# Performance work log

Hardware: AMD Instinct MI355X
Metric: run time of the kernel (lower is better)

Reference implementation:

```python
import jax, jax.numpy as jnp
import numpy as np

B, N, C, P, K = 8, 65536, 96, 96, 512


def _ln(x, g, b, eps=1e-5):
    mu = x.mean(axis=-1, keepdims=True)
    var = ((x - mu) ** 2).mean(axis=-1, keepdims=True)
    return (x - mu) * jax.lax.rsqrt(var + eps) * g + b


def setup_inputs():
    key = jax.random.key(0)
    ks = jax.random.split(key, 8)
    inp = {
        "pts_feat": jax.random.normal(ks[0], (B, N, C), jnp.float32),
        "sp_idx": jax.random.randint(ks[1], (B, N), 0, K, jnp.int64),
        "all_xyz": jax.random.normal(ks[2], (B, N, 3), jnp.float32),
        # pts_proj1: Linear(3,P) -> LN -> ReLU -> Linear(P,P) -> LN
        "W1": jax.random.normal(ks[3], (3, P), jnp.float32) / np.sqrt(3.0),
        "b1": jnp.zeros((P,), jnp.float32),
        "g1": jnp.ones((P,), jnp.float32),
        "be1": jnp.zeros((P,), jnp.float32),
        "W2": jax.random.normal(ks[4], (P, P), jnp.float32) / np.sqrt(P),
        "b2": jnp.zeros((P,), jnp.float32),
        "g2": jnp.ones((P,), jnp.float32),
        "be2": jnp.zeros((P,), jnp.float32),
        # pts_proj2: Linear(2P,P) -> LN -> ReLU -> Linear(P,1,no bias) -> Sigmoid
        "W3": jax.random.normal(ks[5], (2 * P, P), jnp.float32) / np.sqrt(2.0 * P),
        "b3": jnp.zeros((P,), jnp.float32),
        "g3": jnp.ones((P,), jnp.float32),
        "be3": jnp.zeros((P,), jnp.float32),
        "W4": jax.random.normal(ks[6], (P, 1), jnp.float32) / np.sqrt(P),
        "num_sp": K,
    }
    return inp


def reference(pts_feat, sp_idx, all_xyz, W1, b1, g1, be1, W2, b2, g2, be2,
              W3, b3, g3, be3, W4, num_sp):
    Bx, Nx, Cx = pts_feat.shape
    S = Bx * num_sp  # total superpoints across batch (uniform K per batch)
    idx = (sp_idx + jnp.arange(Bx, dtype=sp_idx.dtype)[:, None] * num_sp).reshape(-1)
    xyz = all_xyz.reshape(-1, 3)
    feat = pts_feat.reshape(-1, Cx)

    # scatter_norm: unit-sphere normalize per segment
    mn = jax.ops.segment_min(xyz, idx, num_segments=S)
    mx = jax.ops.segment_max(xyz, idx, num_segments=S)
    cnt = jax.ops.segment_sum(jnp.ones((xyz.shape[0],), xyz.dtype), idx, num_segments=S)
    cnt_c = jnp.maximum(cnt, 1.0)
    center = jax.ops.segment_sum(xyz, idx, num_segments=S) / cnt_c[:, None]
    diam = (mx - mn).max(axis=1)
    pts = (xyz - center[idx]) / (diam[idx][:, None] + 0.01)

    # pts_proj1
    h = _ln(pts @ W1 + b1, g1, be1)
    h = jax.nn.relu(h)
    h = _ln(h @ W2 + b2, g2, be2)

    seg = jax.ops.segment_max(h, idx, num_segments=S)  # (S, P)
    cat = jnp.concatenate([h, seg[idx]], axis=-1)      # (B*N, 2P)

    # pts_proj2
    z = _ln(cat @ W3 + b3, g3, be3)
    z = jax.nn.relu(z)
    w = jax.nn.sigmoid(z @ W4) * 2.0                   # (B*N, 1)

    sp_feat = jax.ops.segment_sum(feat * w, idx, num_segments=S) / cnt_c[:, None] + seg
    return sp_feat.reshape(Bx, num_sp, Cx), w.reshape(Bx, Nx, 1)
```

## Files before the change

### kernel.cpp

```cpp
#include <hip/hip_runtime.h>
#include <cstdint>

#define MM 524288
#define NSEG 4096

#define WS_SCNT   0u
#define WS_CURSOR 4096u
#define WS_OFFS   8192u
#define WS_M1     12288u
#define WS_CENTER 12304u
#define WS_DIAM   24592u
#define WS_SEGF   28688u
#define WS_ZSEG   421904u
#define WS_SORTED 815120u
#define WS_SEG16  1339408u
#define WS_WSRT   1601552u
#define WS_H8     2125840u
#define WS_END    (WS_H8 + 25165824u)

typedef __attribute__((ext_vector_type(8))) short short8;
typedef __attribute__((ext_vector_type(4))) float f32x4;

#define WPAD 104

__device__ __forceinline__ unsigned bfr(float x) {
    unsigned u = __float_as_uint(x);
    return (u + 0x7FFFu + ((u >> 16) & 1u)) >> 16;
}
__device__ __forceinline__ float bf2f(unsigned v) {
    return __uint_as_float(v << 16);
}
union U4S8 { uint4 u; short8 s; };

__global__ void __launch_bounds__(256) k0_init(unsigned* __restrict__ ws)
{
    unsigned i = blockIdx.x * 256u + threadIdx.x;
    if (i < 8192u) ws[i] = 0u;
}

__global__ void __launch_bounds__(256) k1_count(
    const int* __restrict__ spidx, unsigned* __restrict__ scnt)
{
    __shared__ unsigned lcnt[512];
    int tid = threadIdx.x;
    for (int j = tid; j < 512; j += 256) lcnt[j] = 0u;
    __syncthreads();
    int base = blockIdx.x * 4096;
    #pragma unroll 4
    for (int it = 0; it < 16; ++it) {
        int p = base + it*256 + tid;
        atomicAdd(&lcnt[spidx[p]], 1u);
    }
    __syncthreads();
    int b = blockIdx.x >> 4;
    for (int j = tid; j < 512; j += 256)
        atomicAdd(&scnt[(b << 9) + j], lcnt[j]);
}

__global__ void __launch_bounds__(1024) k2_scan(
    const unsigned* __restrict__ scnt, unsigned* __restrict__ offs,
    const float* __restrict__ W1, const float* __restrict__ b1, float* __restrict__ m1)
{
    __shared__ unsigned sh[1024];
    int t = threadIdx.x;
    unsigned c0 = scnt[t*4+0], c1 = scnt[t*4+1], c2 = scnt[t*4+2], c3 = scnt[t*4+3];
    unsigned tot = c0 + c1 + c2 + c3;
    sh[t] = tot;
    __syncthreads();
    for (int d = 1; d < 1024; d <<= 1) {
        unsigned v = (t >= d) ? sh[t-d] : 0u;
        __syncthreads();
        sh[t] += v;
        __syncthreads();
    }
    unsigned excl = sh[t] - tot;
    offs[t*4+0] = excl;
    offs[t*4+1] = excl + c0;
    offs[t*4+2] = excl + c0 + c1;
    offs[t*4+3] = excl + c0 + c1 + c2;

    if (t == 0) {
        float Sa=0,Sb=0,Sc=0,Sd=0,Saa=0,Sbb=0,Scc=0,Sdd=0,Sab=0,Sac=0,Sad=0,Sbc=0,Sbd=0,Scd=0;
        #pragma unroll 8
        for (int j = 0; j < 96; ++j) {
            float A = W1[j], B2 = W1[96+j], C2 = W1[192+j], D = b1[j];
            Sa+=A; Sb+=B2; Sc+=C2; Sd+=D;
            Saa=fmaf(A,A,Saa); Sbb=fmaf(B2,B2,Sbb); Scc=fmaf(C2,C2,Scc); Sdd=fmaf(D,D,Sdd);
            Sab=fmaf(A,B2,Sab); Sac=fmaf(A,C2,Sac); Sad=fmaf(A,D,Sad);
            Sbc=fmaf(B2,C2,Sbc); Sbd=fmaf(B2,D,Sbd); Scd=fmaf(C2,D,Scd);
        }
        const float inv = 1.f/96.f;
        float Am=Sa*inv, Bm=Sb*inv, Cm=Sc*inv, Dm=Sd*inv;
        m1[0]=Am; m1[1]=Bm; m1[2]=Cm; m1[3]=Dm;
        m1[4]=Saa*inv-Am*Am; m1[5]=Sbb*inv-Bm*Bm; m1[6]=Scc*inv-Cm*Cm; m1[7]=Sdd*inv-Dm*Dm;
        m1[8]=Sab*inv-Am*Bm; m1[9]=Sac*inv-Am*Cm; m1[10]=Sad*inv-Am*Dm;
        m1[11]=Sbc*inv-Bm*Cm; m1[12]=Sbd*inv-Bm*Dm; m1[13]=Scd*inv-Cm*Dm;
    }
}

__global__ void __launch_bounds__(256) k3_scatter(
    const int* __restrict__ spidx, const unsigned* __restrict__ offs,
    unsigned* __restrict__ cursor, unsigned* __restrict__ sorted,
    unsigned short* __restrict__ seg16)
{
    __shared__ unsigned lcnt[512];
    __shared__ unsigned gbase[512];
    __shared__ unsigned short rank16[4096];
    int tid = threadIdx.x;
    for (int j = tid; j < 512; j += 256) lcnt[j] = 0u;
    __syncthreads();
    int base = blockIdx.x * 4096;
    #pragma unroll 4
    for (int it = 0; it < 16; ++it) {
        int p = base + it*256 + tid;
        unsigned r = atomicAdd(&lcnt[spidx[p]], 1u);
        rank16[it*256 + tid] = (unsigned short)r;
    }
    __syncthreads();
    int b = blockIdx.x >> 4;
    for (int j = tid; j < 512; j += 256)
        gbase[j] = atomicAdd(&cursor[(b << 9) + j], lcnt[j]);
    __syncthreads();
    #pragma unroll 4
    for (int it = 0; it < 16; ++it) {
        int p = base + it*256 + tid;
        int sl = spidx[p];
        int s = (b << 9) + sl;
        unsigned pos = offs[s] + gbase[sl] + (unsigned)rank16[it*256 + tid];
        sorted[pos] = (unsigned)p;
        seg16[pos] = (unsigned short)s;
    }
}

__global__ void __launch_bounds__(128) k3b_stats(
    const float* __restrict__ xyz, const unsigned* __restrict__ sorted,
    const unsigned* __restrict__ offs, const unsigned* __restrict__ scnt,
    float* __restrict__ center, float* __restrict__ diam)
{
    int s = blockIdx.x, tid = threadIdx.x;
    unsigned cnt = scnt[s], off = offs[s];
    float mnx=INFINITY, mny=INFINITY, mnz=INFINITY;
    float mxx=-INFINITY, mxy=-INFINITY, mxz=-INFINITY;
    float smx=0.f, smy=0.f, smz=0.f;
    for (unsigned r = tid; r < cnt; r += 128) {
        unsigned p = sorted[off + r];
        float x = xyz[3*p], y = xyz[3*p+1], z = xyz[3*p+2];
        mnx = fminf(mnx, x); mny = fminf(mny, y); mnz = fminf(mnz, z);
        mxx = fmaxf(mxx, x); mxy = fmaxf(mxy, y); mxz = fmaxf(mxz, z);
        smx += x; smy += y; smz += z;
    }
    #pragma unroll
    for (int m = 1; m < 64; m <<= 1) {
        mnx = fminf(mnx, __shfl_xor(mnx, m)); mny = fminf(mny, __shfl_xor(mny, m));
        mnz = fminf(mnz, __shfl_xor(mnz, m));
        mxx = fmaxf(mxx, __shfl_xor(mxx, m)); mxy = fmaxf(mxy, __shfl_xor(mxy, m));
        mxz = fmaxf(mxz, __shfl_xor(mxz, m));
        smx += __shfl_xor(smx, m); smy += __shfl_xor(smy, m); smz += __shfl_xor(smz, m);
    }
    __shared__ float cw[2][9];
    if ((tid & 63) == 0) {
        int w = tid >> 6;
        cw[w][0]=mnx; cw[w][1]=mny; cw[w][2]=mnz;
        cw[w][3]=mxx; cw[w][4]=mxy; cw[w][5]=mxz;
        cw[w][6]=smx; cw[w][7]=smy; cw[w][8]=smz;
    }
    __syncthreads();
    if (tid == 0) {
        float a0=fminf(cw[0][0],cw[1][0]), a1=fminf(cw[0][1],cw[1][1]), a2=fminf(cw[0][2],cw[1][2]);
        float b0=fmaxf(cw[0][3],cw[1][3]), b1=fmaxf(cw[0][4],cw[1][4]), b2=fmaxf(cw[0][5],cw[1][5]);
        float s0=cw[0][6]+cw[1][6], s1=cw[0][7]+cw[1][7], s2=cw[0][8]+cw[1][8];
        float cc = fmaxf((float)cnt, 1.f);
        center[s*3+0] = s0/cc; center[s*3+1] = s1/cc; center[s*3+2] = s2/cc;
        diam[s] = fmaxf(fmaxf(b0-a0, b1-a1), b2-a2);
    }
}

__global__ void __launch_bounds__(256) kTA(
    const float* __restrict__ xyz,
    const unsigned* __restrict__ sorted,
    const unsigned short* __restrict__ seg16,
    const float* __restrict__ center, const float* __restrict__ diam,
    const float* __restrict__ W1, const float* __restrict__ b1,
    const float* __restrict__ g1, const float* __restrict__ be1,
    const float* __restrict__ m1,
    const float* __restrict__ W2, const float* __restrict__ b2,
    const float* __restrict__ g2, const float* __restrict__ be2,
    uint4* __restrict__ h8)
{
    __shared__ unsigned short wT[96*WPAD];
    __shared__ float pw[96*6];
    __shared__ float prm[3*96];
    int tid = threadIdx.x;
    #pragma unroll 4
    for (int it = 0; it < 36; ++it) {
        int e = it*256 + tid;
        int i = e / 96, j = e - i*96;
        wT[j*WPAD + i] = (unsigned short)bfr(W2[e]);
    }
    if (tid < 96) {
        pw[tid*6+0] = W1[tid]; pw[tid*6+1] = W1[96+tid]; pw[tid*6+2] = W1[192+tid];
        pw[tid*6+3] = b1[tid]; pw[tid*6+4] = g1[tid];    pw[tid*6+5] = be1[tid];
        prm[tid] = b2[tid]; prm[96+tid] = g2[tid]; prm[192+tid] = be2[tid];
    }
    __syncthreads();

    float mc[14];
    #pragma unroll
    for (int k = 0; k < 14; ++k) mc[k] = m1[k];

    int lane = tid & 63, w = tid >> 6;
    int pcol = lane & 15, g = lane >> 4;
    size_t slot0 = (size_t)blockIdx.x * 256 + w*64 + pcol;

    #pragma unroll 1
    for (int t = 0; t < 4; ++t) {
        size_t slot = slot0 + (size_t)t * 16;
        unsigned p = sorted[slot];
        int s = seg16[slot];
        float dinv = 1.f / (diam[s] + 0.01f);
        float px = (xyz[3*p+0] - center[3*s+0]) * dinv;
        float py = (xyz[3*p+1] - center[3*s+1]) * dinv;
        float pz = (xyz[3*p+2] - center[3*s+2]) * dinv;

        float mu = fmaf(px, mc[0], fmaf(py, mc[1], fmaf(pz, mc[2], mc[3])));
        float var = fmaf(px*px, mc[4], fmaf(py*py, mc[5], fmaf(pz*pz, mc[6], mc[7])));
        var = fmaf(2.f*px*py, mc[8],  var);
        var = fmaf(2.f*px*pz, mc[9],  var);
        var = fmaf(2.f*px,    mc[10], var);
        var = fmaf(2.f*py*pz, mc[11], var);
        var = fmaf(2.f*py,    mc[12], var);
        var = fmaf(2.f*pz,    mc[13], var);
        float rs = rsqrtf(var + 1e-5f);

        U4S8 bu[3];
        #pragma unroll
        for (int ks = 0; ks < 3; ++ks) {
            unsigned vv[4];
            #pragma unroll
            for (int e2 = 0; e2 < 4; ++e2) {
                int i0 = ks*32 + g*8 + e2*2;
                const float* r0 = &pw[i0*6];
                float ta = fmaf(px, r0[0], fmaf(py, r0[1], fmaf(pz, r0[2], r0[3])));
                ta = fmaxf(fmaf((ta - mu) * rs, r0[4], r0[5]), 0.f);
                const float* r1 = &pw[(i0+1)*6];
                float tb = fmaf(px, r1[0], fmaf(py, r1[1], fmaf(pz, r1[2], r1[3])));
                tb = fmaxf(fmaf((tb - mu) * rs, r1[4], r1[5]), 0.f);
                vv[e2] = bfr(ta) | (bfr(tb) << 16);
            }
            bu[ks].u.x = vv[0]; bu[ks].u.y = vv[1]; bu[ks].u.z = vv[2]; bu[ks].u.w = vv[3];
        }

        f32x4 acc[6];
        #pragma unroll
        for (int nt = 0; nt < 6; ++nt) acc[nt] = (f32x4){0.f,0.f,0.f,0.f};

        #pragma unroll
        for (int ks = 0; ks < 3; ++ks) {
            #pragma unroll
            for (int nt = 0; nt < 6; ++nt) {
                const short8 aF = *(const short8*)&wT[(nt*16 + pcol)*WPAD + ks*32 + g*8];
                acc[nt] = __builtin_amdgcn_mfma_f32_16x16x32_bf16(aF, bu[ks].s, acc[nt], 0, 0, 0);
            }
        }

        float sum = 0.f, sq = 0.f;
        #pragma unroll
        for (int nt = 0; nt < 6; ++nt) {
            f32x4 bv = *(const f32x4*)&prm[nt*16 + g*4];
            #pragma unroll
            for (int r = 0; r < 4; ++r) {
                float v = acc[nt][r] + bv[r];
                acc[nt][r] = v;
                sum += v;
                sq = fmaf(v, v, sq);
            }
        }
        sum += __shfl_xor(sum, 16); sum += __shfl_xor(sum, 32);
        sq  += __shfl_xor(sq, 16);  sq  += __shfl_xor(sq, 32);
        float muh = sum * (1.f/96.f);
        float rsh = rsqrtf(sq * (1.f/96.f) - muh*muh + 1e-5f);

        #pragma unroll
        for (int nt = 0; nt < 6; ++nt) {
            f32x4 gv  = *(const f32x4*)&prm[96  + nt*16 + g*4];
            f32x4 bev = *(const f32x4*)&prm[192 + nt*16 + g*4];
            float o0 = fmaf((acc[nt][0]-muh)*rsh, gv[0], bev[0]);
            float o1 = fmaf((acc[nt][1]-muh)*rsh, gv[1], bev[1]);
            float o2 = fmaf((acc[nt][2]-muh)*rsh, gv[2], bev[2]);
            float o3 = fmaf((acc[nt][3]-muh)*rsh, gv[3], bev[3]);
            uint2 st;
            st.x = bfr(o0) | (bfr(o1) << 16);
            st.y = bfr(o2) | (bfr(o3) << 16);
            int j0 = nt*16 + g*4;
            size_t q = (size_t)(nt*2 + (g >> 1));
            *(uint2*)((char*)h8 + (q*MM + slot)*16 + (size_t)(j0 & 7)*2) = st;
        }
    }
}

__global__ void __launch_bounds__(192) kB_seg(
    const uint4* __restrict__ h8,
    const unsigned* __restrict__ offs, const unsigned* __restrict__ scnt,
    const float* __restrict__ W3, const float* __restrict__ b3,
    float* __restrict__ segf, float* __restrict__ zseg)
{
    __shared__ uint4 st[16][13];
    __shared__ float lseg[96];
    int s = blockIdx.x, tid = threadIdx.x;
    unsigned cnt = scnt[s], off = offs[s];
    int r = tid & 15, q = tid >> 4;
    float mx = -INFINITY;
    for (unsigned base = 0; base < cnt; base += 16) {
        uint4 v = make_uint4(0xFF80FF80u, 0xFF80FF80u, 0xFF80FF80u, 0xFF80FF80u);
        if (q < 12 && base + (unsigned)r < cnt)
            v = h8[(size_t)q * MM + off + base + r];
        if (q < 12) st[r][q] = v;
        __syncthreads();
        if (tid < 96) {
            int qj = tid >> 3, ej = tid & 7;
            #pragma unroll
            for (int rr = 0; rr < 16; ++rr) {
                const unsigned short* hp = (const unsigned short*)&st[rr][qj];
                mx = fmaxf(mx, bf2f(hp[ej]));
            }
        }
        __syncthreads();
    }
    if (tid < 96) { segf[(size_t)s*96 + tid] = mx; lseg[tid] = mx; }
    __syncthreads();
    if (tid < 96) {
        float acc = b3[tid];
        #pragma unroll 4
        for (int i = 0; i < 96; ++i)
            acc = fmaf(lseg[i], W3[(size_t)(96+i)*96 + tid], acc);
        zseg[(size_t)s*96 + tid] = acc;
    }
}

__global__ void __launch_bounds__(256) kC_mfma(
    const uint4* __restrict__ h8, const float* __restrict__ zseg,
    const unsigned short* __restrict__ seg16, const unsigned* __restrict__ sorted,
    const float* __restrict__ W3, const float* __restrict__ g3,
    const float* __restrict__ be3, const float* __restrict__ W4,
    float* __restrict__ w_nat, float* __restrict__ w_srt)
{
    __shared__ unsigned short wT[96*WPAD];
    __shared__ float prm[3*96];
    int tid = threadIdx.x;
    #pragma unroll 4
    for (int it = 0; it < 36; ++it) {
        int e = it*256 + tid;
        int i = e / 96, j = e - i*96;
        wT[j*WPAD + i] = (unsigned short)bfr(W3[e]);
    }
    if (tid < 96) { prm[tid] = g3[tid]; prm[96+tid] = be3[tid]; prm[192+tid] = W4[tid]; }
    __syncthreads();

    int lane = tid & 63, w = tid >> 6;
    int pcol = lane & 15, g = lane >> 4;
    size_t slot0 = (size_t)blockIdx.x * 256 + w*64 + pcol;

    #pragma unroll 1
    for (int t = 0; t < 4; ++t) {
        size_t slot = slot0 + (size_t)t * 16;
        U4S8 bu[3];
        #pragma unroll
        for (int ks = 0; ks < 3; ++ks)
            bu[ks].u = h8[(size_t)(ks*4+g) * MM + slot];

        f32x4 acc[6];
        #pragma unroll
        for (int nt = 0; nt < 6; ++nt) acc[nt] = (f32x4){0.f,0.f,0.f,0.f};

        #pragma unroll
        for (int ks = 0; ks < 3; ++ks) {
            #pragma unroll
            for (int nt = 0; nt < 6; ++nt) {
                const short8 aF = *(const short8*)&wT[(nt*16 + pcol)*WPAD + ks*32 + g*8];
                acc[nt] = __builtin_amdgcn_mfma_f32_16x16x32_bf16(aF, bu[ks].s, acc[nt], 0, 0, 0);
            }
        }

        int s = seg16[slot];
        float sum = 0.f, sq = 0.f;
        #pragma unroll
        for (int nt = 0; nt < 6; ++nt) {
            f32x4 zs = *(const f32x4*)&zseg[(size_t)s*96 + nt*16 + g*4];
            #pragma unroll
            for (int r = 0; r < 4; ++r) {
                float v = acc[nt][r] + zs[r];
                acc[nt][r] = v;
                sum += v;
                sq = fmaf(v, v, sq);
            }
        }
        sum += __shfl_xor(sum, 16); sum += __shfl_xor(sum, 32);
        sq  += __shfl_xor(sq, 16);  sq  += __shfl_xor(sq, 32);
        float mu = sum * (1.f/96.f);
        float rs = rsqrtf(sq * (1.f/96.f) - mu*mu + 1e-5f);

        float tt = 0.f;
        #pragma unroll
        for (int nt = 0; nt < 6; ++nt) {
            f32x4 gv  = *(const f32x4*)&prm[nt*16 + g*4];
            f32x4 bev = *(const f32x4*)&prm[96 + nt*16 + g*4];
            f32x4 w4v = *(const f32x4*)&prm[192 + nt*16 + g*4];
            #pragma unroll
            for (int r = 0; r < 4; ++r) {
                float v = fmaxf(fmaf((acc[nt][r]-mu)*rs, gv[r], bev[r]), 0.f);
                tt = fmaf(v, w4v[r], tt);
            }
        }
        tt += __shfl_xor(tt, 16); tt += __shfl_xor(tt, 32);
        if (lane < 16) {
            float wv = 2.f / (1.f + expf(-tt));
            w_srt[slot] = wv;
            w_nat[sorted[slot]] = wv;
        }
    }
}

__global__ void __launch_bounds__(128) kD_pool(
    const float* __restrict__ feat, const float* __restrict__ w_srt,
    const unsigned* __restrict__ sorted, const unsigned* __restrict__ offs,
    const unsigned* __restrict__ scnt, const float* __restrict__ segf,
    float* __restrict__ sp_out)
{
    int s = blockIdx.x;
    int c = threadIdx.x;
    unsigned cnt = scnt[s], off = offs[s];
    float acc = 0.f;
    unsigned r = 0;
    for (; r + 4 <= cnt; r += 4) {
        unsigned p0 = sorted[off+r],   p1 = sorted[off+r+1];
        unsigned p2 = sorted[off+r+2], p3 = sorted[off+r+3];
        float w0 = w_srt[off+r], w1 = w_srt[off+r+1], w2 = w_srt[off+r+2], w3 = w_srt[off+r+3];
        if (c < 96) {
            acc = fmaf(feat[(size_t)p0*96 + c], w0, acc);
            acc = fmaf(feat[(size_t)p1*96 + c], w1, acc);
            acc = fmaf(feat[(size_t)p2*96 + c], w2, acc);
            acc = fmaf(feat[(size_t)p3*96 + c], w3, acc);
        }
    }
    for (; r < cnt; ++r) {
        unsigned p0 = sorted[off+r];
        float w0 = w_srt[off+r];
        if (c < 96) acc = fmaf(feat[(size_t)p0*96 + c], w0, acc);
    }
    if (c < 96) {
        float cc = fmaxf((float)cnt, 1.f);
        sp_out[(size_t)s*96 + c] = acc / cc + segf[(size_t)s*96 + c];
    }
}

extern "C" void kernel_launch(void* const* d_in, const int* in_sizes, int n_in,
                              void* d_out, int out_size, void* d_ws, size_t ws_size,
                              hipStream_t stream)
{
    const float* pts_feat = (const float*)d_in[0];
    const int*   sp_idx   = (const int*)d_in[1];
    const float* xyz      = (const float*)d_in[2];
    const float* W1  = (const float*)d_in[3];
    const float* b1  = (const float*)d_in[4];
    const float* g1  = (const float*)d_in[5];
    const float* be1 = (const float*)d_in[6];
    const float* W2  = (const float*)d_in[7];
    const float* b2  = (const float*)d_in[8];
    const float* g2  = (const float*)d_in[9];
    const float* be2 = (const float*)d_in[10];
    const float* W3  = (const float*)d_in[11];
    const float* b3  = (const float*)d_in[12];
    const float* g3  = (const float*)d_in[13];
    const float* be3 = (const float*)d_in[14];
    const float* W4  = (const float*)d_in[15];

    float* out = (float*)d_out;
    float* sp_out = out;
    float* w_out  = out + (size_t)NSEG * 96;

    if (ws_size < (size_t)WS_END * 4u) return;

    unsigned* ws32   = (unsigned*)d_ws;
    unsigned* scnt   = ws32 + WS_SCNT;
    unsigned* cursor = ws32 + WS_CURSOR;
    unsigned* offs   = ws32 + WS_OFFS;
    float*    m1     = (float*)(ws32 + WS_M1);
    float*    center = (float*)(ws32 + WS_CENTER);
    float*    diam   = (float*)(ws32 + WS_DIAM);
    float*    segf   = (float*)(ws32 + WS_SEGF);
    float*    zseg   = (float*)(ws32 + WS_ZSEG);
    unsigned* sorted = ws32 + WS_SORTED;
    unsigned short* seg16 = (unsigned short*)(ws32 + WS_SEG16);
    float*    w_srt  = (float*)(ws32 + WS_WSRT);
    uint4*    h8     = (uint4*)(ws32 + WS_H8);

    k0_init<<<32, 256, 0, stream>>>(ws32);
    k1_count<<<MM/4096, 256, 0, stream>>>(sp_idx, scnt);
    k2_scan<<<1, 1024, 0, stream>>>(scnt, offs, W1, b1, m1);
    k3_scatter<<<MM/4096, 256, 0, stream>>>(sp_idx, offs, cursor, sorted, seg16);
    k3b_stats<<<NSEG, 128, 0, stream>>>(xyz, sorted, offs, scnt, center, diam);
    kTA<<<MM/256, 256, 0, stream>>>(xyz, sorted, seg16, center, diam,
        W1, b1, g1, be1, m1, W2, b2, g2, be2, h8);
    kB_seg<<<NSEG, 192, 0, stream>>>(h8, offs, scnt, W3, b3, segf, zseg);
    kC_mfma<<<MM/256, 256, 0, stream>>>(h8, zseg, seg16, sorted, W3, g3, be3, W4,
        w_out, w_srt);
    kD_pool<<<NSEG, 128, 0, stream>>>(pts_feat, w_srt, sorted, offs, scnt, segf, sp_out);
}
```

Baseline: 265.0 us.

## Recompute first MLP instead of storing h, fuse segment max via atomics

The bf16 intermediate h buffer (about 100 MB written and read twice) is removed. The first kernel now computes h and reduces the per-segment max in place, using order-preserving uint atomicMax into shared memory and then global memory. The second MLP kernel recomputes h from xyz and transposes it through LDS before the W3 MFMA. This trades extra MFMA and ALU work plus atomic traffic for much less HBM traffic. The pooling loop is also unrolled to 8.

```diff
diff --git a/kernel.cpp b/kernel.cpp
--- a/kernel.cpp
+++ b/kernel.cpp
@@ -10,13 +10,13 @@
 #define WS_M1     12288u
 #define WS_CENTER 12304u
 #define WS_DIAM   24592u
-#define WS_SEGF   28688u
-#define WS_ZSEG   421904u
-#define WS_SORTED 815120u
-#define WS_SEG16  1339408u
-#define WS_WSRT   1601552u
-#define WS_H8     2125840u
-#define WS_END    (WS_H8 + 25165824u)
+#define WS_SEGU   28688u
+#define WS_SEGF   421904u
+#define WS_ZSEG   815120u
+#define WS_SORTED 1208336u
+#define WS_SEG16  1732624u
+#define WS_WSRT   1994768u
+#define WS_END    2519056u
 
 typedef __attribute__((ext_vector_type(8))) short short8;
 typedef __attribute__((ext_vector_type(4))) float f32x4;
@@ -30,12 +30,21 @@
 __device__ __forceinline__ float bf2f(unsigned v) {
     return __uint_as_float(v << 16);
 }
+__device__ __forceinline__ unsigned ford(float f) {
+    unsigned u = __float_as_uint(f);
+    return (u & 0x80000000u) ? ~u : (u | 0x80000000u);
+}
+__device__ __forceinline__ float ford_inv(unsigned e) {
+    unsigned u = (e & 0x80000000u) ? (e & 0x7FFFFFFFu) : ~e;
+    return __uint_as_float(u);
+}
 union U4S8 { uint4 u; short8 s; };
 
 __global__ void __launch_bounds__(256) k0_init(unsigned* __restrict__ ws)
 {
     unsigned i = blockIdx.x * 256u + threadIdx.x;
     if (i < 8192u) ws[i] = 0u;
+    else if (i < 8192u + 393216u) ws[WS_SEGU + i - 8192u] = 0u;
 }
 
 __global__ void __launch_bounds__(256) k1_count(
@@ -175,21 +184,91 @@
     }
 }
 
-__global__ void __launch_bounds__(256) kTA(
+__device__ __forceinline__ void compute_h(
+    float px, float py, float pz, const float* mc,
+    const unsigned short* wT, const float* pw, const float* prm2,
+    int pcol, int g, f32x4 acc[6])
+{
+    float mu = fmaf(px, mc[0], fmaf(py, mc[1], fmaf(pz, mc[2], mc[3])));
+    float var = fmaf(px*px, mc[4], fmaf(py*py, mc[5], fmaf(pz*pz, mc[6], mc[7])));
+    var = fmaf(2.f*px*py, mc[8],  var);
+    var = fmaf(2.f*px*pz, mc[9],  var);
+    var = fmaf(2.f*px,    mc[10], var);
+    var = fmaf(2.f*py*pz, mc[11], var);
+    var = fmaf(2.f*py,    mc[12], var);
+    var = fmaf(2.f*pz,    mc[13], var);
+    float rs = rsqrtf(var + 1e-5f);
+
+    U4S8 bu[3];
+    #pragma unroll
+    for (int ks = 0; ks < 3; ++ks) {
+        unsigned vv[4];
+        #pragma unroll
+        for (int e2 = 0; e2 < 4; ++e2) {
+            int i0 = ks*32 + g*8 + e2*2;
+            const float* r0 = &pw[i0*6];
+            float ta = fmaf(px, r0[0], fmaf(py, r0[1], fmaf(pz, r0[2], r0[3])));
+            ta = fmaxf(fmaf((ta - mu) * rs, r0[4], r0[5]), 0.f);
+            const float* r1 = &pw[(i0+1)*6];
+            float tb = fmaf(px, r1[0], fmaf(py, r1[1], fmaf(pz, r1[2], r1[3])));
+            tb = fmaxf(fmaf((tb - mu) * rs, r1[4], r1[5]), 0.f);
+            vv[e2] = bfr(ta) | (bfr(tb) << 16);
+        }
+        bu[ks].u.x = vv[0]; bu[ks].u.y = vv[1]; bu[ks].u.z = vv[2]; bu[ks].u.w = vv[3];
+    }
+
+    #pragma unroll
+    for (int nt = 0; nt < 6; ++nt) acc[nt] = (f32x4){0.f,0.f,0.f,0.f};
+    #pragma unroll
+    for (int ks = 0; ks < 3; ++ks) {
+        #pragma unroll
+        for (int nt = 0; nt < 6; ++nt) {
+            const short8 aF = *(const short8*)&wT[(nt*16 + pcol)*WPAD + ks*32 + g*8];
+            acc[nt] = __builtin_amdgcn_mfma_f32_16x16x32_bf16(aF, bu[ks].s, acc[nt], 0, 0, 0);
+        }
+    }
+
+    float sum = 0.f, sq = 0.f;
+    #pragma unroll
+    for (int nt = 0; nt < 6; ++nt) {
+        f32x4 bv = *(const f32x4*)&prm2[nt*16 + g*4];
+        #pragma unroll
+        for (int r = 0; r < 4; ++r) {
+            float v = acc[nt][r] + bv[r];
+            acc[nt][r] = v;
+            sum += v;
+            sq = fmaf(v, v, sq);
+        }
+    }
+    sum += __shfl_xor(sum, 16); sum += __shfl_xor(sum, 32);
+    sq  += __shfl_xor(sq, 16);  sq  += __shfl_xor(sq, 32);
+    float muh = sum * (1.f/96.f);
+    float rsh = rsqrtf(sq * (1.f/96.f) - muh*muh + 1e-5f);
+    #pragma unroll
+    for (int nt = 0; nt < 6; ++nt) {
+        f32x4 gv  = *(const f32x4*)&prm2[96  + nt*16 + g*4];
+        f32x4 bev = *(const f32x4*)&prm2[192 + nt*16 + g*4];
+        #pragma unroll
+        for (int r = 0; r < 4; ++r)
+            acc[nt][r] = fmaf((acc[nt][r]-muh)*rsh, gv[r], bev[r]);
+    }
+}
+
+__global__ void __launch_bounds__(256) kS_segmax(
     const float* __restrict__ xyz,
-    const unsigned* __restrict__ sorted,
-    const unsigned short* __restrict__ seg16,
+    const unsigned* __restrict__ sorted, const unsigned short* __restrict__ seg16,
     const float* __restrict__ center, const float* __restrict__ diam,
     const float* __restrict__ W1, const float* __restrict__ b1,
     const float* __restrict__ g1, const float* __restrict__ be1,
     const float* __restrict__ m1,
     const float* __restrict__ W2, const float* __restrict__ b2,
     const float* __restrict__ g2, const float* __restrict__ be2,
-    uint4* __restrict__ h8)
+    unsigned* __restrict__ segu)
 {
     __shared__ unsigned short wT[96*WPAD];
     __shared__ float pw[96*6];
-    __shared__ float prm[3*96];
+    __shared__ float prm2[3*96];
+    __shared__ unsigned lmax[8*96];
     int tid = threadIdx.x;
     #pragma unroll 4
     for (int it = 0; it < 36; ++it) {
@@ -200,8 +279,9 @@
     if (tid < 96) {
         pw[tid*6+0] = W1[tid]; pw[tid*6+1] = W1[96+tid]; pw[tid*6+2] = W1[192+tid];
         pw[tid*6+3] = b1[tid]; pw[tid*6+4] = g1[tid];    pw[tid*6+5] = be1[tid];
-        prm[tid] = b2[tid]; prm[96+tid] = g2[tid]; prm[192+tid] = be2[tid];
-    }
+        prm2[tid] = b2[tid]; prm2[96+tid] = g2[tid]; prm2[192+tid] = be2[tid];
+    }
+    for (int k = tid; k < 768; k += 256) lmax[k] = 0u;
     __syncthreads();
 
     float mc[14];
@@ -211,122 +291,90 @@
     int lane = tid & 63, w = tid >> 6;
     int pcol = lane & 15, g = lane >> 4;
     size_t slot0 = (size_t)blockIdx.x * 256 + w*64 + pcol;
+    int s0 = seg16[(size_t)blockIdx.x * 256];
 
     #pragma unroll 1
     for (int t = 0; t < 4; ++t) {
         size_t slot = slot0 + (size_t)t * 16;
         unsigned p = sorted[slot];
-        int s = seg16[slot];
-        float dinv = 1.f / (diam[s] + 0.01f);
-        float px = (xyz[3*p+0] - center[3*s+0]) * dinv;
-        float py = (xyz[3*p+1] - center[3*s+1]) * dinv;
-        float pz = (xyz[3*p+2] - center[3*s+2]) * dinv;
-
-        float mu = fmaf(px, mc[0], fmaf(py, mc[1], fmaf(pz, mc[2], mc[3])));
-        float var = fmaf(px*px, mc[4], fmaf(py*py, mc[5], fmaf(pz*pz, mc[6], mc[7])));
-        var = fmaf(2.f*px*py, mc[8],  var);
-        var = fmaf(2.f*px*pz, mc[9],  var);
-        var = fmaf(2.f*px,    mc[10], var);
-        var = fmaf(2.f*py*pz, mc[11], var);
-        var = fmaf(2.f*py,    mc[12], var);
-        var = fmaf(2.f*pz,    mc[13], var);
-        float rs = rsqrtf(var + 1e-5f);
-
-        U4S8 bu[3];
-        #pragma unroll
-        for (int ks = 0; ks < 3; ++ks) {
-            unsigned vv[4];
+        int ss = seg16[slot];
+        float dinv = 1.f / (diam[ss] + 0.01f);
+        float px = (xyz[3*p+0] - center[3*ss+0]) * dinv;
+        float py = (xyz[3*p+1] - center[3*ss+1]) * dinv;
+        float pz = (xyz[3*p+2] - center[3*ss+2]) * dinv;
+
+        f32x4 acc[6];
+        compute_h(px, py, pz, mc, wT, pw, prm2, pcol, g, acc);
+
+        int smin = ss, smax = ss;
+        #pragma unroll
+        for (int m = 1; m < 16; m <<= 1) {
+            smin = min(smin, __shfl_xor(smin, m));
+            smax = max(smax, __shfl_xor(smax, m));
+        }
+        if (smin == smax) {
             #pragma unroll
-            for (int e2 = 0; e2 < 4; ++e2) {
-                int i0 = ks*32 + g*8 + e2*2;
-                const float* r0 = &pw[i0*6];
-                float ta = fmaf(px, r0[0], fmaf(py, r0[1], fmaf(pz, r0[2], r0[3])));
-                ta = fmaxf(fmaf((ta - mu) * rs, r0[4], r0[5]), 0.f);
-                const float* r1 = &pw[(i0+1)*6];
-                float tb = fmaf(px, r1[0], fmaf(py, r1[1], fmaf(pz, r1[2], r1[3])));
-                tb = fmaxf(fmaf((tb - mu) * rs, r1[4], r1[5]), 0.f);
-                vv[e2] = bfr(ta) | (bfr(tb) << 16);
+            for (int m = 1; m < 16; m <<= 1)
+                #pragma unroll
+                for (int nt = 0; nt < 6; ++nt)
+                    #pragma unroll
+                    for (int rr = 0; rr < 4; ++rr)
+                        acc[nt][rr] = fmaxf(acc[nt][rr], __shfl_xor(acc[nt][rr], m));
+            if (pcol == 0) {
+                int rel = ss - s0;
+                if (rel < 8) {
+                    #pragma unroll
+                    for (int nt = 0; nt < 6; ++nt)
+                        #pragma unroll
+                        for (int rr = 0; rr < 4; ++rr)
+                            atomicMax(&lmax[rel*96 + nt*16 + g*4 + rr], ford(acc[nt][rr]));
+                } else {
+                    #pragma unroll
+                    for (int nt = 0; nt < 6; ++nt)
+                        #pragma unroll
+                        for (int rr = 0; rr < 4; ++rr)
+                            atomicMax(&segu[(size_t)ss*96 + nt*16 + g*4 + rr], ford(acc[nt][rr]));
+                }
             }
-            bu[ks].u.x = vv[0]; bu[ks].u.y = vv[1]; bu[ks].u.z = vv[2]; bu[ks].u.w = vv[3];
-        }
-
-        f32x4 acc[6];
-        #pragma unroll
-        for (int nt = 0; nt < 6; ++nt) acc[nt] = (f32x4){0.f,0.f,0.f,0.f};
-
-        #pragma unroll
-        for (int ks = 0; ks < 3; ++ks) {
+        } else {
+            int rel = ss - s0;
             #pragma unroll
             for (int nt = 0; nt < 6; ++nt) {
-                const short8 aF = *(const short8*)&wT[(nt*16 + pcol)*WPAD + ks*32 + g*8];
-                acc[nt] = __builtin_amdgcn_mfma_f32_16x16x32_bf16(aF, bu[ks].s, acc[nt], 0, 0, 0);
+                #pragma unroll
+                for (int rr = 0; rr < 4; ++rr) {
+                    unsigned e = ford(acc[nt][rr]);
+                    int j = nt*16 + g*4 + rr;
+                    if (rel < 8) atomicMax(&lmax[rel*96 + j], e);
+                    else         atomicMax(&segu[(size_t)ss*96 + j], e);
+                }
             }
         }
-
-        float sum = 0.f, sq = 0.f;
-        #pragma unroll
-        for (int nt = 0; nt < 6; ++nt) {
-            f32x4 bv = *(const f32x4*)&prm[nt*16 + g*4];
-            #pragma unroll
-            for (int r = 0; r < 4; ++r) {
-                float v = acc[nt][r] + bv[r];
-                acc[nt][r] = v;
-                sum += v;
-                sq = fmaf(v, v, sq);
-            }
-        }
-        sum += __shfl_xor(sum, 16); sum += __shfl_xor(sum, 32);
-        sq  += __shfl_xor(sq, 16);  sq  += __shfl_xor(sq, 32);
-        float muh = sum * (1.f/96.f);
-        float rsh = rsqrtf(sq * (1.f/96.f) - muh*muh + 1e-5f);
-
-        #pragma unroll
-        for (int nt = 0; nt < 6; ++nt) {
-            f32x4 gv  = *(const f32x4*)&prm[96  + nt*16 + g*4];
-            f32x4 bev = *(const f32x4*)&prm[192 + nt*16 + g*4];
-            float o0 = fmaf((acc[nt][0]-muh)*rsh, gv[0], bev[0]);
-            float o1 = fmaf((acc[nt][1]-muh)*rsh, gv[1], bev[1]);
-            float o2 = fmaf((acc[nt][2]-muh)*rsh, gv[2], bev[2]);
-            float o3 = fmaf((acc[nt][3]-muh)*rsh, gv[3], bev[3]);
-            uint2 st;
-            st.x = bfr(o0) | (bfr(o1) << 16);
-            st.y = bfr(o2) | (bfr(o3) << 16);
-            int j0 = nt*16 + g*4;
-            size_t q = (size_t)(nt*2 + (g >> 1));
-            *(uint2*)((char*)h8 + (q*MM + slot)*16 + (size_t)(j0 & 7)*2) = st;
-        }
-    }
-}
-
-__global__ void __launch_bounds__(192) kB_seg(
-    const uint4* __restrict__ h8,
-    const unsigned* __restrict__ offs, const unsigned* __restrict__ scnt,
+    }
+    __syncthreads();
+    for (int k = tid; k < 768; k += 256) {
+        unsigned v = lmax[k];
+        if (v) {
+            int rel = k / 96, j = k - rel*96;
+            int s = s0 + rel;
+            if (s < NSEG) atomicMax(&segu[(size_t)s*96 + j], v);
+        }
+    }
+}
+
+__global__ void __launch_bounds__(128) kZ_seg(
+    const unsigned* __restrict__ segu,
     const float* __restrict__ W3, const float* __restrict__ b3,
     float* __restrict__ segf, float* __restrict__ zseg)
 {
-    __shared__ uint4 st[16][13];
     __shared__ float lseg[96];
     int s = blockIdx.x, tid = threadIdx.x;
-    unsigned cnt = scnt[s], off = offs[s];
-    int r = tid & 15, q = tid >> 4;
-    float mx = -INFINITY;
-    for (unsigned base = 0; base < cnt; base += 16) {
-        uint4 v = make_uint4(0xFF80FF80u, 0xFF80FF80u, 0xFF80FF80u, 0xFF80FF80u);
-        if (q < 12 && base + (unsigned)r < cnt)
-            v = h8[(size_t)q * MM + off + base + r];
-        if (q < 12) st[r][q] = v;
-        __syncthreads();
-        if (tid < 96) {
-            int qj = tid >> 3, ej = tid & 7;
-            #pragma unroll
-            for (int rr = 0; rr < 16; ++rr) {
-                const unsigned short* hp = (const unsigned short*)&st[rr][qj];
-                mx = fmaxf(mx, bf2f(hp[ej]));
-            }
-        }
-        __syncthreads();
-    }
-    if (tid < 96) { segf[(size_t)s*96 + tid] = mx; lseg[tid] = mx; }
+    if (tid < 96) {
+        unsigned raw = segu[(size_t)s*96 + tid];
+        if (raw == 0u) raw = 0x007FFFFFu;
+        float v = ford_inv(raw);
+        segf[(size_t)s*96 + tid] = v;
+        lseg[tid] = v;
+    }
     __syncthreads();
     if (tid < 96) {
         float acc = b3[tid];
@@ -337,59 +385,98 @@
     }
 }
 
-__global__ void __launch_bounds__(256) kC_mfma(
-    const uint4* __restrict__ h8, const float* __restrict__ zseg,
-    const unsigned short* __restrict__ seg16, const unsigned* __restrict__ sorted,
+__global__ void __launch_bounds__(256) kC_mlp2(
+    const float* __restrict__ xyz,
+    const unsigned* __restrict__ sorted, const unsigned short* __restrict__ seg16,
+    const float* __restrict__ center, const float* __restrict__ diam,
+    const float* __restrict__ W1, const float* __restrict__ b1,
+    const float* __restrict__ g1, const float* __restrict__ be1,
+    const float* __restrict__ m1,
+    const float* __restrict__ W2, const float* __restrict__ b2,
+    const float* __restrict__ g2, const float* __restrict__ be2,
+    const float* __restrict__ zseg,
     const float* __restrict__ W3, const float* __restrict__ g3,
     const float* __restrict__ be3, const float* __restrict__ W4,
     float* __restrict__ w_nat, float* __restrict__ w_srt)
 {
-    __shared__ unsigned short wT[96*WPAD];
-    __shared__ float prm[3*96];
+    __shared__ unsigned short wT2[96*WPAD];
+    __shared__ unsigned short wT3[96*WPAD];
+    __shared__ float pw[96*6];
+    __shared__ float prm2[3*96];
+    __shared__ float prm3[3*96];
+    __shared__ __align__(16) unsigned short tbuf[4][16*104];
     int tid = threadIdx.x;
     #pragma unroll 4
     for (int it = 0; it < 36; ++it) {
         int e = it*256 + tid;
         int i = e / 96, j = e - i*96;
-        wT[j*WPAD + i] = (unsigned short)bfr(W3[e]);
-    }
-    if (tid < 96) { prm[tid] = g3[tid]; prm[96+tid] = be3[tid]; prm[192+tid] = W4[tid]; }
-    __syncthreads();
+        wT2[j*WPAD + i] = (unsigned short)bfr(W2[e]);
+        wT3[j*WPAD + i] = (unsigned short)bfr(W3[e]);
+    }
+    if (tid < 96) {
+        pw[tid*6+0] = W1[tid]; pw[tid*6+1] = W1[96+tid]; pw[tid*6+2] = W1[192+tid];
+        pw[tid*6+3] = b1[tid]; pw[tid*6+4] = g1[tid];    pw[tid*6+5] = be1[tid];
+        prm2[tid] = b2[tid]; prm2[96+tid] = g2[tid]; prm2[192+tid] = be2[tid];
+        prm3[tid] = g3[tid]; prm3[96+tid] = be3[tid]; prm3[192+tid] = W4[tid];
+    }
+    __syncthreads();
+
+    float mc[14];
+    #pragma unroll
+    for (int k = 0; k < 14; ++k) mc[k] = m1[k];
 
     int lane = tid & 63, w = tid >> 6;
     int pcol = lane & 15, g = lane >> 4;
     size_t slot0 = (size_t)blockIdx.x * 256 + w*64 + pcol;
+    unsigned short* tb = &tbuf[w][0];
 
     #pragma unroll 1
     for (int t = 0; t < 4; ++t) {
         size_t slot = slot0 + (size_t)t * 16;
-        U4S8 bu[3];
+        unsigned p = sorted[slot];
+        int ss = seg16[slot];
+        float dinv = 1.f / (diam[ss] + 0.01f);
+        float px = (xyz[3*p+0] - center[3*ss+0]) * dinv;
+        float py = (xyz[3*p+1] - center[3*ss+1]) * dinv;
+        float pz = (xyz[3*p+2] - center[3*ss+2]) * dinv;
+
+        f32x4 acc[6];
+        compute_h(px, py, pz, mc, wT2, pw, prm2, pcol, g, acc);
+
+        #pragma unroll
+        for (int nt = 0; nt < 6; ++nt) {
+            uint2 st;
+            st.x = bfr(acc[nt][0]) | (bfr(acc[nt][1]) << 16);
+            st.y = bfr(acc[nt][2]) | (bfr(acc[nt][3]) << 16);
+            *(uint2*)&tb[pcol*104 + nt*16 + g*4] = st;
+        }
+        __syncthreads();
+        U4S8 hb[3];
         #pragma unroll
         for (int ks = 0; ks < 3; ++ks)
-            bu[ks].u = h8[(size_t)(ks*4+g) * MM + slot];
-
-        f32x4 acc[6];
-        #pragma unroll
-        for (int nt = 0; nt < 6; ++nt) acc[nt] = (f32x4){0.f,0.f,0.f,0.f};
-
+            hb[ks].u = *(const uint4*)&tb[pcol*104 + ks*32 + g*8];
+        __syncthreads();
+
+        f32x4 a2[6];
+        #pragma unroll
+        for (int nt = 0; nt < 6; ++nt) a2[nt] = (f32x4){0.f,0.f,0.f,0.f};
         #pragma unroll
         for (int ks = 0; ks < 3; ++ks) {
             #pragma unroll
             for (int nt = 0; nt < 6; ++nt) {
-                const short8 aF = *(const short8*)&wT[(nt*16 + pcol)*WPAD + ks*32 + g*8];
-                acc[nt] = __builtin_amdgcn_mfma_f32_16x16x32_bf16(aF, bu[ks].s, acc[nt], 0, 0, 0);
+                const short8 aF = *(const short8*)&wT3[(nt*16 + pcol)*WPAD + ks*32 + g*8];
+                a2[nt] = __builtin_amdgcn_mfma_f32_16x16x32_bf16(aF, hb[ks].s, a2[nt], 0, 0, 0);
             }
         }
 
-        int s = seg16[slot];
         float sum = 0.f, sq = 0.f;
         #pragma unroll
         for (int nt = 0; nt < 6; ++nt) {
-            f32x4 zs = *(const f32x4*)&zseg[(size_t)s*96 + nt*16 + g*4];
+            f32x4 zs = *(const f32x4*)&zseg[(size_t)ss*96 + nt*16 + g*4];
             #pragma unroll
             for (int r = 0; r < 4; ++r) {
-                float v = acc[nt][r] + zs[r];
-                acc[nt][r] = v;
+                float v = a2[nt][r] + zs[r];
+                a2[nt][r] = v;
                 sum += v;
                 sq = fmaf(v, v, sq);
             }
@@ -402,12 +489,12 @@
         float tt = 0.f;
         #pragma unroll
         for (int nt = 0; nt < 6; ++nt) {
-            f32x4 gv  = *(const f32x4*)&prm[nt*16 + g*4];
-            f32x4 bev = *(const f32x4*)&prm[96 + nt*16 + g*4];
-            f32x4 w4v = *(const f32x4*)&prm[192 + nt*16 + g*4];
+            f32x4 gv  = *(const f32x4*)&prm3[nt*16 + g*4];
+            f32x4 bev = *(const f32x4*)&prm3[96 + nt*16 + g*4];
+            f32x4 w4v = *(const f32x4*)&prm3[192 + nt*16 + g*4];
             #pragma unroll
             for (int r = 0; r < 4; ++r) {
-                float v = fmaxf(fmaf((acc[nt][r]-mu)*rs, gv[r], bev[r]), 0.f);
+                float v = fmaxf(fmaf((a2[nt][r]-mu)*rs, gv[r], bev[r]), 0.f);
                 tt = fmaf(v, w4v[r], tt);
             }
         }
@@ -415,7 +502,7 @@
         if (lane < 16) {
             float wv = 2.f / (1.f + expf(-tt));
             w_srt[slot] = wv;
-            w_nat[sorted[slot]] = wv;
+            w_nat[p] = wv;
         }
     }
 }
@@ -431,20 +518,22 @@
     unsigned cnt = scnt[s], off = offs[s];
     float acc = 0.f;
     unsigned r = 0;
-    for (; r + 4 <= cnt; r += 4) {
-        unsigned p0 = sorted[off+r],   p1 = sorted[off+r+1];
-        unsigned p2 = sorted[off+r+2], p3 = sorted[off+r+3];
-        float w0 = w_srt[off+r], w1 = w_srt[off+r+1], w2 = w_srt[off+r+2], w3 = w_srt[off+r+3];
+    for (; r + 8 <= cnt; r += 8) {
+        unsigned pp[8]; float ww[8];
+        #pragma unroll
+        for (int k = 0; k < 8; ++k) {
+            pp[k] = sorted[off + r + k];
+            ww[k] = w_srt[off + r + k];
+        }
         if (c < 96) {
-            acc = fmaf(feat[(size_t)p0*96 + c], w0, acc);
-            acc = fmaf(feat[(size_t)p1*96 + c], w1, acc);
-            acc = fmaf(feat[(size_t)p2*96 + c], w2, acc);
-            acc = fmaf(feat[(size_t)p3*96 + c], w3, acc);
+            #pragma unroll
+            for (int k = 0; k < 8; ++k)
+                acc = fmaf(feat[(size_t)pp[k]*96 + c], ww[k], acc);
         }
     }
     for (; r < cnt; ++r) {
-        unsigned p0 = sorted[off+r];
-        float w0 = w_srt[off+r];
+        unsigned p0 = sorted[off + r];
+        float w0 = w_srt[off + r];
         if (c < 96) acc = fmaf(feat[(size_t)p0*96 + c], w0, acc);
     }
     if (c < 96) {
@@ -487,22 +576,22 @@
     float*    m1     = (float*)(ws32 + WS_M1);
     float*    center = (float*)(ws32 + WS_CENTER);
     float*    diam   = (float*)(ws32 + WS_DIAM);
+    unsigned* segu   = ws32 + WS_SEGU;
     float*    segf   = (float*)(ws32 + WS_SEGF);
     float*    zseg   = (float*)(ws32 + WS_ZSEG);
     unsigned* sorted = ws32 + WS_SORTED;
     unsigned short* seg16 = (unsigned short*)(ws32 + WS_SEG16);
     float*    w_srt  = (float*)(ws32 + WS_WSRT);
-    uint4*    h8     = (uint4*)(ws32 + WS_H8);
-
-    k0_init<<<32, 256, 0, stream>>>(ws32);
+
+    k0_init<<<1568, 256, 0, stream>>>(ws32);
     k1_count<<<MM/4096, 256, 0, stream>>>(sp_idx, scnt);
     k2_scan<<<1, 1024, 0, stream>>>(scnt, offs, W1, b1, m1);
     k3_scatter<<<MM/4096, 256, 0, stream>>>(sp_idx, offs, cursor, sorted, seg16);
     k3b_stats<<<NSEG, 128, 0, stream>>>(xyz, sorted, offs, scnt, center, diam);
-    kTA<<<MM/256, 256, 0, stream>>>(xyz, sorted, seg16, center, diam,
-        W1, b1, g1, be1, m1, W2, b2, g2, be2, h8);
-    kB_seg<<<NSEG, 192, 0, stream>>>(h8, offs, scnt, W3, b3, segf, zseg);
-    kC_mfma<<<MM/256, 256, 0, stream>>>(h8, zseg, seg16, sorted, W3, g3, be3, W4,
-        w_out, w_srt);
+    kS_segmax<<<MM/256, 256, 0, stream>>>(xyz, sorted, seg16, center, diam,
+        W1, b1, g1, be1, m1, W2, b2, g2, be2, segu);
+    kZ_seg<<<NSEG, 128, 0, stream>>>(segu, W3, b3, segf, zseg);
+    kC_mlp2<<<MM/256, 256, 0, stream>>>(xyz, sorted, seg16, center, diam,
+        W1, b1, g1, be1, m1, W2, b2, g2, be2, zseg, W3, g3, be3, W4, w_out, w_srt);
     kD_pool<<<NSEG, 128, 0, stream>>>(pts_feat, w_srt, sorted, offs, scnt, segf, sp_out);
 }
```

After: 339.1 us. 1.28x slower.
